# Kernel optimization log

Hardware: AMD Instinct MI355X
Metric: run time of the kernel (lower is better)

Reference implementation:

```python
import jax, jax.numpy as jnp
from jax import lax
import numpy as np

T = 100  # number of binarization thresholds, as in nn.Module (linspace(0,1,100))
THRESHOLDS = jnp.linspace(0.0, 1.0, T)


def _count_components(binimg):
    """4-connected component count per image via iterative min-label propagation.
    binimg: [N,H,W] float in {0,1}. Returns [N] int32 component counts.
    Equivalent math to the source's recursive DFS flood fill, vectorized."""
    N, H, W = binimg.shape
    fg = binimg > 0
    BIG = H * W  # sentinel label for background
    idx = jnp.arange(H * W, dtype=jnp.int32).reshape(H, W)
    lab0 = jnp.where(fg, idx[None], jnp.int32(BIG))

    def prop(lab):
        p = jnp.pad(lab, ((0, 0), (1, 1), (1, 1)), constant_values=BIG)
        nmin = jnp.minimum(jnp.minimum(p[:, :-2, 1:-1], p[:, 2:, 1:-1]),
                           jnp.minimum(p[:, 1:-1, :-2], p[:, 1:-1, 2:]))
        return jnp.where(fg, jnp.minimum(lab, nmin), jnp.int32(BIG))

    def cond(c):
        return ~c[1]

    def body(c):
        lab = c[0]
        new = prop(prop(prop(lab)))  # 3 propagation steps per convergence check
        return (new, jnp.all(new == lab))

    lab, _ = lax.while_loop(cond, body, (lab0, jnp.array(False)))
    # each component keeps exactly one pixel whose label equals its own index
    return jnp.sum(fg & (lab == idx[None]), axis=(1, 2)).astype(jnp.int32)


def _betti(prob):
    """prob: [R,H,W] -> [T,R,2] (b0, b1) per threshold per region.
    b1 = b0 - euler, euler = #pixels - #4-neighbor edges (as in source)."""
    R, H, W = prob.shape
    binz = (prob[None] > THRESHOLDS[:, None, None, None]).astype(jnp.float32)  # [T,R,H,W]
    flat = binz.reshape(T * R, H, W)
    b0 = lax.stop_gradient(_count_components(flat)).astype(jnp.float32).reshape(T, R)
    pix = flat.sum((1, 2))
    edges = (flat[:, :-1] * flat[:, 1:]).sum((1, 2)) + (flat[:, :, :-1] * flat[:, :, 1:]).sum((1, 2))
    euler = (pix - edges).reshape(T, R)
    b1 = b0 - euler
    return jnp.stack([b0, b1], axis=-1)  # [T,R,2]


def setup_inputs() -> dict:
    key = jax.random.key(0)
    k1, k2 = jax.random.split(key)
    three_class_prob = jax.random.uniform(k1, (4, 3, 128, 128), dtype=jnp.float32)
    selected_regions = jnp.arange(4, dtype=jnp.int64)
    gt_barcodes = jax.random.uniform(k2, (4, 6, T - 1, 2), dtype=jnp.float32)
    return {"three_class_prob": three_class_prob,
            "selected_regions": selected_regions,
            "gt_barcodes": gt_barcodes}


def reference(three_class_prob, selected_regions, gt_barcodes):
    sel = three_class_prob[selected_regions]  # [R,3,H,W]
    inside = _betti(sel[:, 0])     # channel 0
    boundary = _betti(sel[:, 1])   # channel 1
    union = inside                 # source uses channel 0:1 again -> same values
    codes = jnp.concatenate([inside, boundary, union], axis=-1)  # [T,R,6]
    # barcode extraction: birth at increases of the betti curve, death at decreases
    d = codes[1:] - codes[:-1]                 # [T-1,R,6]
    th = THRESHOLDS[:-1, None, None]
    birth = jnp.where(d > 0, th, 0.0)
    death = jnp.where(d < 0, th, 0.0)
    barcodes = jnp.stack([birth, death], axis=-1).transpose(1, 2, 0, 3)  # [R,6,T-1,2]
    # fixed-shape matching: pair barcodes sorted by birth time (Hungarian surrogate)
    ord_b = jnp.argsort(barcodes[..., 0], axis=-1)
    ord_g = jnp.argsort(gt_barcodes[..., 0], axis=-1)
    bs = jnp.take_along_axis(barcodes, ord_b[..., None], axis=-2)
    gs = jnp.take_along_axis(gt_barcodes, ord_g[..., None], axis=-2)
    matched_diff = jnp.sum(jnp.abs(bs - gs), axis=-1)                  # [R,6,T-1]
    unmatched_len = jnp.sum(barcodes[..., 1] - barcodes[..., 0], axis=-1)  # [R,6]
    return jnp.mean(matched_diff) + jnp.mean(unmatched_len)
```

## Files before the change

### kernel.cpp

```cpp
#include <hip/hip_runtime.h>

#define NPIX 16384
#define IMW  128

__device__ __forceinline__ int find_root(int* L, int a){
    int p = L[a];
    while(p != a){
        int gp = L[p];
        if(gp != p) L[a] = gp;
        a = p; p = gp;
    }
    return a;
}

__device__ __forceinline__ void unite(int* L, int a, int b){
    while(true){
        a = find_root(L, a);
        b = find_root(L, b);
        if(a == b) return;
        int hi = (a > b) ? a : b;
        int lo = (a > b) ? b : a;
        int old = atomicCAS(&L[hi], hi, lo);
        if(old == hi) return;
        a = old; b = lo;
    }
}

__global__ __launch_bounds__(256) void ccl_kernel(const float* __restrict__ prob,
                                                  const int*   __restrict__ sel,
                                                  float*       __restrict__ betti){
    __shared__ unsigned long long M[256];
    __shared__ unsigned long long S[256];
    __shared__ int L[8192];
    __shared__ int red[12];
    const int tid = threadIdx.x, bid = blockIdx.x;
    const int ch = bid / 400, t = (bid % 400) >> 2, r = bid & 3;
    const float th = (float)t / 99.0f;
    const float* img = prob + (size_t)(sel[r] * 3 + ch) * NPIX;

    {
        int4* L4 = (int4*)L;
        for(int i = tid; i < 2048; i += 256){ int b = i * 4; L4[i] = make_int4(b, b+1, b+2, b+3); }
    }

    const int lane = tid & 63, wave = tid >> 6;
    for(int c = 0; c < 64; c++){
        float v = img[c * 256 + wave * 64 + lane];
        unsigned long long mm = __ballot(v > th);
        if(lane == 0) M[c * 4 + wave] = mm;
    }
    __syncthreads();

    const int w = tid, row = w >> 1, half = w & 1;
    const unsigned long long m = M[w];
    const unsigned long long lcar = half ? (M[w - 1] >> 63) : 0ULL;
    const unsigned long long s = m & ~((m << 1) | lcar);
    S[w] = s;
    int pix   = __popcll(m);
    int edges = __popcll(m & ((m << 1) | lcar));
    const unsigned long long va = (row > 0) ? M[w - 2] : 0ULL;
    edges += __popcll(m & va);
    __syncthreads();

    const int base = half ? __popcll(S[w - 1]) : 0;
    if(row > 0){
        unsigned long long c = m & va;
        const unsigned long long ccar = half ? ((M[w - 1] & M[w - 3]) >> 63) : 0ULL;
        unsigned long long cs = c & ~((c << 1) | ccar);
        const unsigned long long sa = S[w - 2];
        const int basea = half ? __popcll(S[w - 3]) : 0;
        while(cs){
            const int x = __ffsll(cs) - 1;
            cs &= cs - 1;
            const unsigned long long lm = (2ULL << x) - 1;
            const int na = (row - 1) * 64 + basea + __popcll(sa & lm) - 1;
            const int nb =  row      * 64 + base  + __popcll(s  & lm) - 1;
            unite(L, na, nb);
        }
    }
    __syncthreads();

    int b0 = 0;
    {   const int nrun = __popcll(s);
        for(int j = 0; j < nrun; j++){ const int n = row * 64 + base + j; b0 += (L[n] == n); } }

    for(int off = 32; off; off >>= 1){
        pix   += __shfl_down(pix,   off, 64);
        edges += __shfl_down(edges, off, 64);
        b0    += __shfl_down(b0,    off, 64);
    }
    if(lane == 0){ red[wave*3] = pix; red[wave*3+1] = edges; red[wave*3+2] = b0; }
    __syncthreads();
    if(tid == 0){
        int P = 0, E = 0, B = 0;
        for(int k = 0; k < 4; k++){ P += red[k*3]; E += red[k*3+1]; B += red[k*3+2]; }
        const float b0f = (float)B;
        const float b1f = b0f - ((float)P - (float)E);
        const size_t o = (((size_t)ch * 100 + t) * 4 + r) * 2;
        betti[o] = b0f; betti[o + 1] = b1f;
    }
}

__global__ __launch_bounds__(128) void rows_kernel(const float* __restrict__ betti,
                                                   const float* __restrict__ gt,
                                                   float*       __restrict__ out){
    __shared__ float codes[100];
    __shared__ float birth[99], bs0[99], bs1[99], gs0[99], gs1[99];
    __shared__ float gsh[198];
    __shared__ float red[4];
    const int row = blockIdx.x;
    const int r = row / 6, j = row % 6;
    const int chmap[6] = {0, 0, 1, 1, 0, 0};
    const int ch = chmap[j], comp = j & 1;
    const int tid = threadIdx.x;

    if(tid < 100) codes[tid] = betti[(((size_t)ch * 100 + tid) * 4 + r) * 2 + comp];
    const float* g = gt + (size_t)row * 99 * 2;
    for(int i = tid; i < 198; i += 128) gsh[i] = g[i];
    __syncthreads();

    float b = 0.f, d = 0.f;
    if(tid < 99){
        const float dv = codes[tid + 1] - codes[tid];
        const float thv = (float)tid / 99.0f;
        b = (dv > 0.f) ? thv : 0.f;
        d = (dv < 0.f) ? thv : 0.f;
        birth[tid] = b;
    }
    __syncthreads();

    if(tid < 99){
        int zb = 0, tz = 0;
        for(int k = 0; k < 99; k++){
            const int z = (birth[k] == 0.f) ? 1 : 0;
            tz += z;
            if(k < tid) zb += z;
        }
        const int pos = (b == 0.f) ? zb : (tz + tid - zb);
        bs0[pos] = b; bs1[pos] = d;

        const float gb = gsh[tid * 2];
        int rank = 0;
        for(int k = 0; k < 99; k++){
            const float o = gsh[k * 2];
            rank += (o < gb || (o == gb && k < tid)) ? 1 : 0;
        }
        gs0[rank] = gb; gs1[rank] = gsh[tid * 2 + 1];
    }
    __syncthreads();

    float mm = 0.f, u = 0.f;
    if(tid < 99){
        mm = fabsf(bs0[tid] - gs0[tid]) + fabsf(bs1[tid] - gs1[tid]);
        u = d - b;
    }
    for(int off = 32; off; off >>= 1){
        mm += __shfl_down(mm, off, 64);
        u  += __shfl_down(u,  off, 64);
    }
    if((tid & 63) == 0){ red[(tid >> 6)*2] = mm; red[(tid >> 6)*2 + 1] = u; }
    __syncthreads();
    if(tid == 0)
        atomicAdd(out, (red[0] + red[2]) / 2376.0f + (red[1] + red[3]) / 24.0f);
}

extern "C" void kernel_launch(void* const* d_in, const int* in_sizes, int n_in,
                              void* d_out, int out_size, void* d_ws, size_t ws_size,
                              hipStream_t stream){
    const float* prob = (const float*)d_in[0];
    const int*   sel  = (const int*)d_in[1];
    const float* gt   = (const float*)d_in[2];
    float* betti = (float*)d_ws;

    hipMemsetAsync(d_out, 0, sizeof(float), stream);
    ccl_kernel <<<800, 256, 0, stream>>>(prob, sel, betti);
    rows_kernel<<<24, 128, 0, stream>>>(betti, gt, (float*)d_out);
}
```

Measured before the change: 105.6 us.

## Fuse CCL and barcode-loss kernels via last-block-done atomic counter

The per-row barcode matching kernel is folded into the CCL kernel. Each block publishes its Betti values, and an atomic counter picks the last block to finish. That block runs all 24 rows serially (two rows at a time across 256 threads) and writes the loss directly. This removes one kernel launch and the memset of the output. In exchange, the tail work becomes serial on a single block, and every block now pays for an agent-scope atomic.

```diff
diff --git a/kernel.cpp b/kernel.cpp
--- a/kernel.cpp
+++ b/kernel.cpp
@@ -26,13 +26,19 @@
     }
 }
 
-__global__ __launch_bounds__(256) void ccl_kernel(const float* __restrict__ prob,
-                                                  const int*   __restrict__ sel,
-                                                  float*       __restrict__ betti){
+__global__ __launch_bounds__(256) void fused_kernel(const float* __restrict__ prob,
+                                                    const int*   __restrict__ sel,
+                                                    const float* __restrict__ gt,
+                                                    unsigned*    __restrict__ cnt,
+                                                    float*       __restrict__ betti,
+                                                    float*       __restrict__ out){
     __shared__ unsigned long long M[256];
     __shared__ unsigned long long S[256];
     __shared__ int L[8192];
     __shared__ int red[12];
+    __shared__ float fred[8];
+    __shared__ int lastFlag;
+
     const int tid = threadIdx.x, bid = blockIdx.x;
     const int ch = bid / 400, t = (bid % 400) >> 2, r = bid & 3;
     const float th = (float)t / 99.0f;
@@ -97,71 +103,85 @@
         const float b0f = (float)B;
         const float b1f = b0f - ((float)P - (float)E);
         const size_t o = (((size_t)ch * 100 + t) * 4 + r) * 2;
-        betti[o] = b0f; betti[o + 1] = b1f;
-    }
-}
-
-__global__ __launch_bounds__(128) void rows_kernel(const float* __restrict__ betti,
-                                                   const float* __restrict__ gt,
-                                                   float*       __restrict__ out){
-    __shared__ float codes[100];
-    __shared__ float birth[99], bs0[99], bs1[99], gs0[99], gs1[99];
-    __shared__ float gsh[198];
-    __shared__ float red[4];
-    const int row = blockIdx.x;
-    const int r = row / 6, j = row % 6;
-    const int chmap[6] = {0, 0, 1, 1, 0, 0};
-    const int ch = chmap[j], comp = j & 1;
-    const int tid = threadIdx.x;
-
-    if(tid < 100) codes[tid] = betti[(((size_t)ch * 100 + tid) * 4 + r) * 2 + comp];
-    const float* g = gt + (size_t)row * 99 * 2;
-    for(int i = tid; i < 198; i += 128) gsh[i] = g[i];
-    __syncthreads();
-
-    float b = 0.f, d = 0.f;
-    if(tid < 99){
-        const float dv = codes[tid + 1] - codes[tid];
-        const float thv = (float)tid / 99.0f;
-        b = (dv > 0.f) ? thv : 0.f;
-        d = (dv < 0.f) ? thv : 0.f;
-        birth[tid] = b;
+        __hip_atomic_store(&betti[o],     b0f, __ATOMIC_RELAXED, __HIP_MEMORY_SCOPE_AGENT);
+        __hip_atomic_store(&betti[o + 1], b1f, __ATOMIC_RELAXED, __HIP_MEMORY_SCOPE_AGENT);
+        const unsigned old = __hip_atomic_fetch_add(cnt, 1u, __ATOMIC_ACQ_REL, __HIP_MEMORY_SCOPE_AGENT);
+        lastFlag = (old == 799u);
     }
     __syncthreads();
+    if(!lastFlag) return;
 
-    if(tid < 99){
-        int zb = 0, tz = 0;
-        for(int k = 0; k < 99; k++){
-            const int z = (birth[k] == 0.f) ? 1 : 0;
-            tz += z;
-            if(k < tid) zb += z;
+    float* RB = (float*)L;
+    const int sub = tid >> 7, lt = tid & 127;
+    float* codes = RB + sub * 800;
+    float* birth = codes + 100;
+    float* bs0   = codes + 199;
+    float* bs1   = codes + 298;
+    float* gs0   = codes + 397;
+    float* gs1   = codes + 496;
+    float* gsh   = codes + 595;
+    const int chmap[6] = {0, 0, 1, 1, 0, 0};
+
+    float msum = 0.f, usum = 0.f;
+    for(int chunk = 0; chunk < 12; chunk++){
+        const int rowi = chunk * 2 + sub;
+        const int rr = rowi / 6, j = rowi % 6;
+        const int cch = chmap[j], comp = j & 1;
+        if(lt < 100)
+            codes[lt] = __hip_atomic_load(&betti[(((size_t)cch * 100 + lt) * 4 + rr) * 2 + comp],
+                                          __ATOMIC_RELAXED, __HIP_MEMORY_SCOPE_AGENT);
+        const float* g = gt + (size_t)rowi * 198;
+        for(int i = lt; i < 198; i += 128) gsh[i] = g[i];
+        __syncthreads();
+
+        float b = 0.f, d = 0.f;
+        if(lt < 99){
+            const float dv = codes[lt + 1] - codes[lt];
+            const float thv = (float)lt / 99.0f;
+            b = (dv > 0.f) ? thv : 0.f;
+            d = (dv < 0.f) ? thv : 0.f;
+            birth[lt] = b;
         }
-        const int pos = (b == 0.f) ? zb : (tz + tid - zb);
-        bs0[pos] = b; bs1[pos] = d;
+        __syncthreads();
 
-        const float gb = gsh[tid * 2];
-        int rank = 0;
-        for(int k = 0; k < 99; k++){
-            const float o = gsh[k * 2];
-            rank += (o < gb || (o == gb && k < tid)) ? 1 : 0;
+        if(lt < 99){
+            int zb = 0, tz = 0;
+            for(int k = 0; k < 99; k++){
+                const int z = (birth[k] == 0.f) ? 1 : 0;
+                tz += z;
+                if(k < lt) zb += z;
+            }
+            const int pos = (b == 0.f) ? zb : (tz + lt - zb);
+            bs0[pos] = b; bs1[pos] = d;
+
+            const float gb = gsh[lt * 2];
+            int rank = 0;
+            for(int k = 0; k < 99; k++){
+                const float o2 = gsh[k * 2];
+                rank += (o2 < gb || (o2 == gb && k < lt)) ? 1 : 0;
+            }
+            gs0[rank] = gb; gs1[rank] = gsh[lt * 2 + 1];
         }
-        gs0[rank] = gb; gs1[rank] = gsh[tid * 2 + 1];
+        __syncthreads();
+
+        if(lt < 99){
+            msum += fabsf(bs0[lt] - gs0[lt]) + fabsf(bs1[lt] - gs1[lt]);
+            usum += d - b;
+        }
+        __syncthreads();
     }
+
+    for(int off = 32; off; off >>= 1){
+        msum += __shfl_down(msum, off, 64);
+        usum += __shfl_down(usum, off, 64);
+    }
+    if((tid & 63) == 0){ fred[(tid >> 6) * 2] = msum; fred[(tid >> 6) * 2 + 1] = usum; }
     __syncthreads();
-
-    float mm = 0.f, u = 0.f;
-    if(tid < 99){
-        mm = fabsf(bs0[tid] - gs0[tid]) + fabsf(bs1[tid] - gs1[tid]);
-        u = d - b;
+    if(tid == 0){
+        const float mm = fred[0] + fred[2] + fred[4] + fred[6];
+        const float uu = fred[1] + fred[3] + fred[5] + fred[7];
+        out[0] = mm / 2376.0f + uu / 24.0f;
     }
-    for(int off = 32; off; off >>= 1){
-        mm += __shfl_down(mm, off, 64);
-        u  += __shfl_down(u,  off, 64);
-    }
-    if((tid & 63) == 0){ red[(tid >> 6)*2] = mm; red[(tid >> 6)*2 + 1] = u; }
-    __syncthreads();
-    if(tid == 0)
-        atomicAdd(out, (red[0] + red[2]) / 2376.0f + (red[1] + red[3]) / 24.0f);
 }
 
 extern "C" void kernel_launch(void* const* d_in, const int* in_sizes, int n_in,
@@ -170,9 +190,9 @@
     const float* prob = (const float*)d_in[0];
     const int*   sel  = (const int*)d_in[1];
     const float* gt   = (const float*)d_in[2];
-    float* betti = (float*)d_ws;
+    unsigned* cnt   = (unsigned*)d_ws;
+    float*    betti = (float*)d_ws + 8;
 
-    hipMemsetAsync(d_out, 0, sizeof(float), stream);
-    ccl_kernel <<<800, 256, 0, stream>>>(prob, sel, betti);
-    rows_kernel<<<24, 128, 0, stream>>>(betti, gt, (float*)d_out);
+    hipMemsetAsync(d_ws, 0, sizeof(unsigned), stream);
+    fused_kernel<<<800, 256, 0, stream>>>(prob, sel, gt, cnt, betti, (float*)d_out);
 }
```

New measurement: 176.3 us. 1.67x slower.

## Load-balance union operations across threads via prefix scan and remove memset launch

Applied to the files above, without the earlier changes.

Flattens the per-row union work into a global list using a wave prefix-sum over per-word connection counts, so each thread handles evenly distributed unite calls found by binary search instead of serially looping over one word's connections. Root counting now scans the whole label array, and b0 is derived as roots minus unused slots plus runs. The output zeroing is moved into the first kernel, removing the separate memset. This costs extra scans, a binary search per union and a full-array root count.

```diff
diff --git a/kernel.cpp b/kernel.cpp
--- a/kernel.cpp
+++ b/kernel.cpp
@@ -1,7 +1,7 @@
 #include <hip/hip_runtime.h>
 
 #define NPIX 16384
-#define IMW  128
+typedef unsigned long long u64;
 
 __device__ __forceinline__ int find_root(int* L, int a){
     int p = L[a];
@@ -28,74 +28,105 @@
 
 __global__ __launch_bounds__(256) void ccl_kernel(const float* __restrict__ prob,
                                                   const int*   __restrict__ sel,
-                                                  float*       __restrict__ betti){
-    __shared__ unsigned long long M[256];
-    __shared__ unsigned long long S[256];
+                                                  float*       __restrict__ betti,
+                                                  float*       __restrict__ out){
+    __shared__ u64 M[256];
+    __shared__ u64 S[256];
+    __shared__ u64 CS[256];
     __shared__ int L[8192];
-    __shared__ int red[12];
+    __shared__ int P[257];
+    __shared__ int red[16];
     const int tid = threadIdx.x, bid = blockIdx.x;
+    if(bid == 0 && tid == 0) atomicExch(out, 0.0f);
     const int ch = bid / 400, t = (bid % 400) >> 2, r = bid & 3;
     const float th = (float)t / 99.0f;
     const float* img = prob + (size_t)(sel[r] * 3 + ch) * NPIX;
 
     {
-        int4* L4 = (int4*)L;
-        for(int i = tid; i < 2048; i += 256){ int b = i * 4; L4[i] = make_int4(b, b+1, b+2, b+3); }
+        int2* L2 = (int2*)L;
+        for(int i = tid; i < 4096; i += 256) L2[i] = make_int2(2*i, 2*i + 1);
     }
 
     const int lane = tid & 63, wave = tid >> 6;
     for(int c = 0; c < 64; c++){
         float v = img[c * 256 + wave * 64 + lane];
-        unsigned long long mm = __ballot(v > th);
+        u64 mm = __ballot(v > th);
         if(lane == 0) M[c * 4 + wave] = mm;
     }
     __syncthreads();
 
     const int w = tid, row = w >> 1, half = w & 1;
-    const unsigned long long m = M[w];
-    const unsigned long long lcar = half ? (M[w - 1] >> 63) : 0ULL;
-    const unsigned long long s = m & ~((m << 1) | lcar);
+    const u64 m = M[w];
+    const u64 lcar = half ? (M[w - 1] >> 63) : 0ULL;
+    const u64 s = m & ~((m << 1) | lcar);
     S[w] = s;
     int pix   = __popcll(m);
     int edges = __popcll(m & ((m << 1) | lcar));
-    const unsigned long long va = (row > 0) ? M[w - 2] : 0ULL;
+    const u64 va = (row > 0) ? M[w - 2] : 0ULL;
     edges += __popcll(m & va);
-    __syncthreads();
-
-    const int base = half ? __popcll(S[w - 1]) : 0;
+    u64 csm = 0ULL;
     if(row > 0){
-        unsigned long long c = m & va;
-        const unsigned long long ccar = half ? ((M[w - 1] & M[w - 3]) >> 63) : 0ULL;
-        unsigned long long cs = c & ~((c << 1) | ccar);
-        const unsigned long long sa = S[w - 2];
-        const int basea = half ? __popcll(S[w - 3]) : 0;
-        while(cs){
-            const int x = __ffsll(cs) - 1;
-            cs &= cs - 1;
-            const unsigned long long lm = (2ULL << x) - 1;
-            const int na = (row - 1) * 64 + basea + __popcll(sa & lm) - 1;
-            const int nb =  row      * 64 + base  + __popcll(s  & lm) - 1;
-            unite(L, na, nb);
-        }
-    }
-    __syncthreads();
-
-    int b0 = 0;
-    {   const int nrun = __popcll(s);
-        for(int j = 0; j < nrun; j++){ const int n = row * 64 + base + j; b0 += (L[n] == n); } }
-
+        const u64 c = m & va;
+        const u64 ccar = half ? ((M[w - 1] & M[w - 3]) >> 63) : 0ULL;
+        csm = c & ~((c << 1) | ccar);
+    }
+    CS[w] = csm;
+    const int cw   = __popcll(csm);
+    const int runs = __popcll(s);
+
+    int incl = cw;
+    for(int off = 1; off < 64; off <<= 1){
+        int n = __shfl_up(incl, off, 64);
+        if(lane >= off) incl += n;
+    }
+    if(lane == 63) red[wave] = incl;
+    __syncthreads();
+    int woff = 0;
+    for(int k = 0; k < wave; k++) woff += red[k];
+    const int excl = woff + incl - cw;
+    P[w] = excl;
+    if(w == 255) P[256] = excl + cw;
+    __syncthreads();
+    const int C = P[256];
+
+    for(int j = tid; j < C; j += 256){
+        int lo = 0, hi = 256;
+        #pragma unroll
+        for(int itv = 0; itv < 8; itv++){ int mid = (lo + hi) >> 1; if(P[mid] <= j) lo = mid; else hi = mid; }
+        const int ww = lo, k = j - P[ww];
+        u64 cs = CS[ww];
+        for(int q = 0; q < k; q++) cs &= cs - 1;
+        const int x = __ffsll(cs) - 1;
+        const u64 lm = (2ULL << x) - 1;
+        const int rw = ww >> 1, hf = ww & 1;
+        const int base  = hf ? __popcll(S[ww - 1]) : 0;
+        const int basea = hf ? __popcll(S[ww - 3]) : 0;
+        const int nb =  rw      * 64 + base  + __popcll(S[ww]     & lm) - 1;
+        const int na = (rw - 1) * 64 + basea + __popcll(S[ww - 2] & lm) - 1;
+        unite(L, na, nb);
+    }
+    __syncthreads();
+
+    int rc = 0;
+    const int2* L2c = (const int2*)L;
+    for(int i = tid; i < 4096; i += 256){ int2 v2 = L2c[i]; rc += (v2.x == 2*i) + (v2.y == 2*i + 1); }
+
+    int v0 = pix, v1 = edges, v2 = runs, v3 = rc;
     for(int off = 32; off; off >>= 1){
-        pix   += __shfl_down(pix,   off, 64);
-        edges += __shfl_down(edges, off, 64);
-        b0    += __shfl_down(b0,    off, 64);
-    }
-    if(lane == 0){ red[wave*3] = pix; red[wave*3+1] = edges; red[wave*3+2] = b0; }
+        v0 += __shfl_down(v0, off, 64);
+        v1 += __shfl_down(v1, off, 64);
+        v2 += __shfl_down(v2, off, 64);
+        v3 += __shfl_down(v3, off, 64);
+    }
+    __syncthreads();
+    if(lane == 0){ red[wave*4] = v0; red[wave*4+1] = v1; red[wave*4+2] = v2; red[wave*4+3] = v3; }
     __syncthreads();
     if(tid == 0){
-        int P = 0, E = 0, B = 0;
-        for(int k = 0; k < 4; k++){ P += red[k*3]; E += red[k*3+1]; B += red[k*3+2]; }
+        int Pp = 0, E = 0, R = 0, RC = 0;
+        for(int k2 = 0; k2 < 4; k2++){ Pp += red[k2*4]; E += red[k2*4+1]; R += red[k2*4+2]; RC += red[k2*4+3]; }
+        const int B = RC - 8192 + R;
         const float b0f = (float)B;
-        const float b1f = b0f - ((float)P - (float)E);
+        const float b1f = b0f - ((float)Pp - (float)E);
         const size_t o = (((size_t)ch * 100 + t) * 4 + r) * 2;
         betti[o] = b0f; betti[o + 1] = b1f;
     }
@@ -172,7 +203,6 @@
     const float* gt   = (const float*)d_in[2];
     float* betti = (float*)d_ws;
 
-    hipMemsetAsync(d_out, 0, sizeof(float), stream);
-    ccl_kernel <<<800, 256, 0, stream>>>(prob, sel, betti);
+    ccl_kernel <<<800, 256, 0, stream>>>(prob, sel, betti, (float*)d_out);
     rows_kernel<<<24, 128, 0, stream>>>(betti, gt, (float*)d_out);
 }
```

Result: slower. 119.8 us (+13.5%).
